# Kernel optimization log

Measured on AMD Instinct MI355X. Metric: run time of the kernel, lower is better.

## Reference

```python
import jax, jax.numpy as jnp
import numpy as np

N = 500_000        # atoms
P = 16_000_000     # neighbor pairs (half list)
NS = 4             # species types
CUTOFF = 2.5
BOX = 20.0         # cubic box edge length


def setup_inputs() -> dict:
    key = jax.random.key(0)
    k = jax.random.split(key, 6)
    positions = jax.random.uniform(k[0], (N, 3), dtype=jnp.float32) * BOX
    cell = jnp.eye(3, dtype=jnp.float32) * BOX
    pair_i = jax.random.randint(k[1], (P,), 0, N, dtype=jnp.int32)
    # guarantee j != i so r2 > 0 even when shift == 0
    offs = jax.random.randint(k[2], (P,), 1, N, dtype=jnp.int32)
    pair_j = (pair_i + offs) % N
    shifts = jax.random.randint(k[3], (P, 3), 0, 3, dtype=jnp.int32)
    species = jax.random.randint(k[4], (N,), 0, NS, dtype=jnp.int32)
    # per-species-pair LJ parameter tables (symmetric), mirroring the
    # dict {(a,b): (sigma, epsilon)} precomputation in __init__
    sig = 0.8 + 0.1 * jnp.arange(NS, dtype=jnp.float32)
    eps = 0.5 + 0.1 * jnp.arange(NS, dtype=jnp.float32)
    sigma_tab = 0.5 * (sig[:, None] + sig[None, :])
    eps_tab = jnp.sqrt(eps[:, None] * eps[None, :])
    sr = sigma_tab / CUTOFF
    shift_tab = 4.0 * eps_tab * (sr ** 12 - sr ** 6)
    return dict(positions=positions, cell=cell, sigma_tab=sigma_tab,
                eps_tab=eps_tab, shift_tab=shift_tab, species=species,
                pair_i=pair_i, pair_j=pair_j, shifts=shifts)


def reference(positions, cell, sigma_tab, eps_tab, shift_tab,
              species, pair_i, pair_j, shifts):
    # gather species-pair params (vectorized dict lookup)
    si = species[pair_i]
    sj = species[pair_j]
    sigma = sigma_tab[si, sj]        # [P]
    epsilon = eps_tab[si, sj]        # [P]
    shift_e = shift_tab[si, sj]      # [P]
    # displacement with periodic cell shift: r_j - r_i + S @ cell
    d = positions[pair_j] - positions[pair_i] + shifts.astype(positions.dtype) @ cell  # [P,3]
    r2 = jnp.sum(d * d, axis=-1)     # [P]
    r6 = r2 * r2 * r2
    sigma3 = sigma * sigma * sigma
    sigma6 = sigma3 * sigma3
    sr6 = sigma6 / r6
    sr12 = sr6 * sr6
    e = 4.0 * epsilon * (sr12 - sr6) - shift_e   # [P]
    # per-atom energy: half to each endpoint (per_atom=True path)
    energy = jnp.zeros(positions.shape[0], dtype=positions.dtype)
    energy = energy.at[pair_i].add(0.5 * e).at[pair_j].add(0.5 * e)
    return energy
```

## Files before the change

### kernel.cpp

```cpp
#include <hip/hip_runtime.h>


#define BUCKET_SHIFT 11
#define BUCKET_SIZE  2048
#define QSCALE       2048.0f
#define QINV         (1.0f / 2048.0f)

#define A_THREADS 512
#define A_PAIRS   8

typedef int vint4 __attribute__((ext_vector_type(4)));

__global__ void lj_zero_kernel(float* __restrict__ out, long n) {
    long i = (long)blockIdx.x * blockDim.x + threadIdx.x;
    if (i < n) out[i] = 0.0f;
}

__global__ void lj_pack8_kernel(const float* __restrict__ pos,
                                const int* __restrict__ species,
                                unsigned long long* __restrict__ tab8,
                                int* __restrict__ cursor,
                                int nb, int cap, int n) {
    int i = blockIdx.x * blockDim.x + threadIdx.x;
    if (i < n) {
        unsigned int ux = (unsigned int)(pos[3 * i]     * QSCALE + 0.5f) & 0xFFFFu;
        unsigned int uy = (unsigned int)(pos[3 * i + 1] * QSCALE + 0.5f) & 0xFFFFu;
        unsigned int uz = (unsigned int)(pos[3 * i + 2] * QSCALE + 0.5f) & 0xFFFFu;
        unsigned long long w = (unsigned long long)ux
                             | ((unsigned long long)uy << 16)
                             | ((unsigned long long)uz << 32)
                             | ((unsigned long long)(species[i] & 3) << 48);
        tab8[i] = w;
    }
    if (i < nb) cursor[i] = i * cap;
}

__global__ void lj_pack_kernel(const float* __restrict__ pos,
                               const int* __restrict__ species,
                               float4* __restrict__ packed, int n) {
    int i = blockIdx.x * blockDim.x + threadIdx.x;
    if (i < n) {
        float4 p;
        p.x = pos[3 * i];
        p.y = pos[3 * i + 1];
        p.z = pos[3 * i + 2];
        p.w = __int_as_float(species[i]);
        packed[i] = p;
    }
}

__device__ __forceinline__ unsigned int lj_encode(float he) {
    unsigned int u = __float_as_uint(he);
    return (u + 0x400u) & 0xFFFFF800u;
}

__global__ __launch_bounds__(A_THREADS) void lj_passA_kernel(
    const unsigned long long* __restrict__ tab8,
    const float* __restrict__ cell,
    const float* __restrict__ sigma_tab,
    const float* __restrict__ eps_tab,
    const float* __restrict__ shift_tab,
    const int* __restrict__ pair_i,
    const int* __restrict__ pair_j,
    const int* __restrict__ shifts,
    unsigned int* __restrict__ record_buf,
    int* __restrict__ cursor,
    int cap, int nb, int P)
{
    __shared__ float s_sig6[16];
    __shared__ float s_eps4[16];
    __shared__ float s_shift[16];
    __shared__ float s_cell[9];
    __shared__ int hist[256];
    __shared__ int basev[256];
    __shared__ int bbase[256];
    __shared__ unsigned int staged[A_THREADS * A_PAIRS * 2];
    __shared__ unsigned char bucketOf[A_THREADS * A_PAIRS * 2];
    int t = threadIdx.x;
    if (t < 16) {
        float s = sigma_tab[t];
        float s3 = s * s * s;
        s_sig6[t] = s3 * s3;
        s_eps4[t] = 4.0f * eps_tab[t];
        s_shift[t] = shift_tab[t];
    }
    if (t < 9) s_cell[t] = cell[t];
    if (t < 256) hist[t] = 0;
    __syncthreads();

    float c00 = s_cell[0], c01 = s_cell[1], c02 = s_cell[2];
    float c10 = s_cell[3], c11 = s_cell[4], c12 = s_cell[5];
    float c20 = s_cell[6], c21 = s_cell[7], c22 = s_cell[8];

    long base = (long)(blockIdx.x * (long)A_THREADS + t) * A_PAIRS;

    unsigned int encI[A_PAIRS], encJ[A_PAIRS];
    int slotij[A_PAIRS];
    int bkt[A_PAIRS];
    int vmask = 0;

    if (base + (A_PAIRS - 1) < P) {
        vmask = (1 << A_PAIRS) - 1;
        vint4 piA = *(const vint4*)(pair_i + base);
        vint4 piB = *(const vint4*)(pair_i + base + 4);
        vint4 pjA = *(const vint4*)(pair_j + base);
        vint4 pjB = *(const vint4*)(pair_j + base + 4);
        int pis[A_PAIRS] = {piA[0], piA[1], piA[2], piA[3], piB[0], piB[1], piB[2], piB[3]};
        int pjs[A_PAIRS] = {pjA[0], pjA[1], pjA[2], pjA[3], pjB[0], pjB[1], pjB[2], pjB[3]};

        unsigned long long gi[A_PAIRS], gj[A_PAIRS];
#pragma unroll
        for (int k = 0; k < A_PAIRS; ++k) {
            gi[k] = tab8[pis[k]];
            gj[k] = tab8[pjs[k]];
        }

        vint4 s0 = *(const vint4*)(shifts + base * 3);
        vint4 s1 = *(const vint4*)(shifts + base * 3 + 4);
        vint4 s2 = *(const vint4*)(shifts + base * 3 + 8);
        vint4 s3 = *(const vint4*)(shifts + base * 3 + 12);
        vint4 s4 = *(const vint4*)(shifts + base * 3 + 16);
        vint4 s5 = *(const vint4*)(shifts + base * 3 + 20);
        int shv[24] = {s0[0], s0[1], s0[2], s0[3], s1[0], s1[1], s1[2], s1[3],
                       s2[0], s2[1], s2[2], s2[3], s3[0], s3[1], s3[2], s3[3],
                       s4[0], s4[1], s4[2], s4[3], s5[0], s5[1], s5[2], s5[3]};

#pragma unroll
        for (int k = 0; k < A_PAIRS; ++k) {
            float fx = (float)shv[3 * k], fy = (float)shv[3 * k + 1], fz = (float)shv[3 * k + 2];
            unsigned long long wi = gi[k], wj = gj[k];
            int xi = (int)(wi & 0xFFFFu), yi = (int)((wi >> 16) & 0xFFFFu), zi = (int)((wi >> 32) & 0xFFFFu);
            int xj = (int)(wj & 0xFFFFu), yj = (int)((wj >> 16) & 0xFFFFu), zj = (int)((wj >> 32) & 0xFFFFu);
            float dlx = (float)(xj - xi) * QINV;
            float dly = (float)(yj - yi) * QINV;
            float dlz = (float)(zj - zi) * QINV;
            float dx = dlx + fx * c00 + fy * c10 + fz * c20;
            float dy = dly + fx * c01 + fy * c11 + fz * c21;
            float dz = dlz + fx * c02 + fy * c12 + fz * c22;
            float r2 = dx * dx + dy * dy + dz * dz;
            float r6 = r2 * r2 * r2;
            int idx = (int)(wi >> 48) * 4 + (int)(wj >> 48);
            float sr6 = s_sig6[idx] / r6;
            float sr12 = sr6 * sr6;
            float he = 0.5f * (s_eps4[idx] * (sr12 - sr6) - s_shift[idx]);
            unsigned int u = lj_encode(he);
            encI[k] = u | (unsigned int)(pis[k] & (BUCKET_SIZE - 1));
            encJ[k] = u | (unsigned int)(pjs[k] & (BUCKET_SIZE - 1));
            bkt[k] = (pis[k] >> BUCKET_SHIFT) | ((pjs[k] >> BUCKET_SHIFT) << 8);
        }
    } else {
#pragma unroll
        for (int k = 0; k < A_PAIRS; ++k) {
            long p = base + k;
            encI[k] = 0; encJ[k] = 0; bkt[k] = 0;
            if (p < P) {
                vmask |= (1 << k);
                int i = pair_i[p], j = pair_j[p];
                float fx = (float)shifts[3 * p], fy = (float)shifts[3 * p + 1], fz = (float)shifts[3 * p + 2];
                unsigned long long wi = tab8[i];
                unsigned long long wj = tab8[j];
                int xi = (int)(wi & 0xFFFFu), yi = (int)((wi >> 16) & 0xFFFFu), zi = (int)((wi >> 32) & 0xFFFFu);
                int xj = (int)(wj & 0xFFFFu), yj = (int)((wj >> 16) & 0xFFFFu), zj = (int)((wj >> 32) & 0xFFFFu);
                float dlx = (float)(xj - xi) * QINV;
                float dly = (float)(yj - yi) * QINV;
                float dlz = (float)(zj - zi) * QINV;
                float dx = dlx + fx * c00 + fy * c10 + fz * c20;
                float dy = dly + fx * c01 + fy * c11 + fz * c21;
                float dz = dlz + fx * c02 + fy * c12 + fz * c22;
                float r2 = dx * dx + dy * dy + dz * dz;
                float r6 = r2 * r2 * r2;
                int idx = (int)(wi >> 48) * 4 + (int)(wj >> 48);
                float sr6 = s_sig6[idx] / r6;
                float sr12 = sr6 * sr6;
                float he = 0.5f * (s_eps4[idx] * (sr12 - sr6) - s_shift[idx]);
                unsigned int u = lj_encode(he);
                encI[k] = u | (unsigned int)(i & (BUCKET_SIZE - 1));
                encJ[k] = u | (unsigned int)(j & (BUCKET_SIZE - 1));
                bkt[k] = (i >> BUCKET_SHIFT) | ((j >> BUCKET_SHIFT) << 8);
            }
        }
    }

#pragma unroll
    for (int k = 0; k < A_PAIRS; ++k) {
        if (vmask & (1 << k)) {
            int si = atomicAdd(&hist[bkt[k] & 255], 1);
            int sj = atomicAdd(&hist[(bkt[k] >> 8) & 255], 1);
            slotij[k] = si | (sj << 16);
        } else {
            slotij[k] = 0;
        }
    }
    __syncthreads();

    if (t < 64) {
        int b0 = t * 4;
        int h0 = hist[b0], h1 = hist[b0 + 1], h2 = hist[b0 + 2], h3 = hist[b0 + 3];
        int s = h0 + h1 + h2 + h3;
        int incl = s;
#pragma unroll
        for (int d = 1; d < 64; d <<= 1) {
            int v = __shfl_up(incl, d, 64);
            if (t >= d) incl += v;
        }
        int excl = incl - s;
        bbase[b0]     = excl;
        bbase[b0 + 1] = excl + h0;
        bbase[b0 + 2] = excl + h0 + h1;
        bbase[b0 + 3] = excl + h0 + h1 + h2;
    }
    if (t < nb) {
        int h = hist[t];
        basev[t] = (h > 0) ? atomicAdd(&cursor[t], h) : 0;
    }
    __syncthreads();

#pragma unroll
    for (int k = 0; k < A_PAIRS; ++k) {
        if (vmask & (1 << k)) {
            int bi = bkt[k] & 255;
            int li = bbase[bi] + (slotij[k] & 0xFFFF);
            staged[li] = encI[k];
            bucketOf[li] = (unsigned char)bi;
            int bj = (bkt[k] >> 8) & 255;
            int lj = bbase[bj] + (slotij[k] >> 16);
            staged[lj] = encJ[k];
            bucketOf[lj] = (unsigned char)bj;
        }
    }
    __syncthreads();

    int total = bbase[255] + hist[255];
    for (int idx = t; idx < total; idx += A_THREADS) {
        int b = (int)bucketOf[idx];
        int g = basev[b] + (idx - bbase[b]);
        if (g < (b + 1) * cap) record_buf[g] = staged[idx];
    }
}

__global__ __launch_bounds__(1024) void lj_passB1_kernel(
    const unsigned int* __restrict__ record_buf,
    const int* __restrict__ cursor,
    float* __restrict__ energy,
    int cap, int N)
{
    __shared__ float e[BUCKET_SIZE];
    int b = blockIdx.x;
    int t = threadIdx.x;
    e[t] = 0.0f;
    e[t + 1024] = 0.0f;
    __syncthreads();

    int begin = b * cap;
    int count = cursor[b] - begin;
    if (count > cap) count = cap;

    int full = count >> 3;
    for (int g = t; g < full; g += 1024) {
        const unsigned int* rp = record_buf + begin + g * 8;
        vint4 a = *(const vint4*)(rp);
        vint4 c = *(const vint4*)(rp + 4);
        unsigned int w0 = (unsigned int)a[0], w1 = (unsigned int)a[1];
        unsigned int w2 = (unsigned int)a[2], w3 = (unsigned int)a[3];
        unsigned int w4 = (unsigned int)c[0], w5 = (unsigned int)c[1];
        unsigned int w6 = (unsigned int)c[2], w7 = (unsigned int)c[3];
        atomicAdd(&e[w0 & 2047u], __uint_as_float(w0 & 0xFFFFF800u));
        atomicAdd(&e[w1 & 2047u], __uint_as_float(w1 & 0xFFFFF800u));
        atomicAdd(&e[w2 & 2047u], __uint_as_float(w2 & 0xFFFFF800u));
        atomicAdd(&e[w3 & 2047u], __uint_as_float(w3 & 0xFFFFF800u));
        atomicAdd(&e[w4 & 2047u], __uint_as_float(w4 & 0xFFFFF800u));
        atomicAdd(&e[w5 & 2047u], __uint_as_float(w5 & 0xFFFFF800u));
        atomicAdd(&e[w6 & 2047u], __uint_as_float(w6 & 0xFFFFF800u));
        atomicAdd(&e[w7 & 2047u], __uint_as_float(w7 & 0xFFFFF800u));
    }
    for (int r = (full << 3) + t; r < count; r += 1024) {
        unsigned int w = record_buf[begin + r];
        atomicAdd(&e[w & 2047u], __uint_as_float(w & 0xFFFFF800u));
    }
    __syncthreads();

    long i0 = (long)b * BUCKET_SIZE + t;
    if (i0 < N) energy[i0] = e[t];
    if (i0 + 1024 < N) energy[i0 + 1024] = e[t + 1024];
}

__device__ __forceinline__ void lj_one_pair_packed(
    int i, int j, float fx, float fy, float fz,
    const float4* __restrict__ packed,
    const float* s_sig6, const float* s_eps4, const float* s_shift,
    float c00, float c01, float c02,
    float c10, float c11, float c12,
    float c20, float c21, float c22,
    float* __restrict__ energy)
{
    float4 gi = packed[i];
    float4 gj = packed[j];
    float dx = gj.x - gi.x + fx * c00 + fy * c10 + fz * c20;
    float dy = gj.y - gi.y + fx * c01 + fy * c11 + fz * c21;
    float dz = gj.z - gi.z + fx * c02 + fy * c12 + fz * c22;
    float r2 = dx * dx + dy * dy + dz * dz;
    float r6 = r2 * r2 * r2;
    int idx = __float_as_int(gi.w) * 4 + __float_as_int(gj.w);
    float sr6 = s_sig6[idx] / r6;
    float sr12 = sr6 * sr6;
    float he = 0.5f * (s_eps4[idx] * (sr12 - sr6) - s_shift[idx]);
    atomicAdd(energy + i, he);
    atomicAdd(energy + j, he);
}

__global__ __launch_bounds__(256) void lj_pairs_packed_kernel(
    const float4* __restrict__ packed,
    const float* __restrict__ cell,
    const float* __restrict__ sigma_tab,
    const float* __restrict__ eps_tab,
    const float* __restrict__ shift_tab,
    const int* __restrict__ pair_i,
    const int* __restrict__ pair_j,
    const int* __restrict__ shifts,
    float* __restrict__ energy,
    int P)
{
    __shared__ float s_sig6[16];
    __shared__ float s_eps4[16];
    __shared__ float s_shift[16];
    __shared__ float s_cell[9];
    int t = threadIdx.x;
    if (t < 16) {
        float s = sigma_tab[t];
        float s3 = s * s * s;
        s_sig6[t] = s3 * s3;
        s_eps4[t] = 4.0f * eps_tab[t];
        s_shift[t] = shift_tab[t];
    }
    if (t < 9) s_cell[t] = cell[t];
    __syncthreads();

    float c00 = s_cell[0], c01 = s_cell[1], c02 = s_cell[2];
    float c10 = s_cell[3], c11 = s_cell[4], c12 = s_cell[5];
    float c20 = s_cell[6], c21 = s_cell[7], c22 = s_cell[8];

    long base = (long)(blockIdx.x * (long)blockDim.x + t) * 4;
    if (base + 3 < P) {
        int4 pi4 = *(const int4*)(pair_i + base);
        int4 pj4 = *(const int4*)(pair_j + base);
        int4 sA = *(const int4*)(shifts + base * 3);
        int4 sB = *(const int4*)(shifts + base * 3 + 4);
        int4 sC = *(const int4*)(shifts + base * 3 + 8);
        int pis[4] = {pi4.x, pi4.y, pi4.z, pi4.w};
        int pjs[4] = {pj4.x, pj4.y, pj4.z, pj4.w};
        int shv[12] = {sA.x, sA.y, sA.z, sA.w, sB.x, sB.y, sB.z, sB.w,
                       sC.x, sC.y, sC.z, sC.w};
#pragma unroll
        for (int k = 0; k < 4; ++k) {
            lj_one_pair_packed(pis[k], pjs[k],
                        (float)shv[3 * k], (float)shv[3 * k + 1], (float)shv[3 * k + 2],
                        packed, s_sig6, s_eps4, s_shift,
                        c00, c01, c02, c10, c11, c12, c20, c21, c22, energy);
        }
    } else {
        for (long p = base; p < P; ++p) {
            lj_one_pair_packed(pair_i[p], pair_j[p],
                        (float)shifts[3 * p], (float)shifts[3 * p + 1], (float)shifts[3 * p + 2],
                        packed, s_sig6, s_eps4, s_shift,
                        c00, c01, c02, c10, c11, c12, c20, c21, c22, energy);
        }
    }
}

__device__ __forceinline__ void lj_one_pair(
    int i, int j, float fx, float fy, float fz,
    const float* __restrict__ pos,
    const int* __restrict__ species,
    const float* s_sig6, const float* s_eps4, const float* s_shift,
    float c00, float c01, float c02,
    float c10, float c11, float c12,
    float c20, float c21, float c22,
    float* __restrict__ energy)
{
    float dx = pos[3 * j]     - pos[3 * i]     + fx * c00 + fy * c10 + fz * c20;
    float dy = pos[3 * j + 1] - pos[3 * i + 1] + fx * c01 + fy * c11 + fz * c21;
    float dz = pos[3 * j + 2] - pos[3 * i + 2] + fx * c02 + fy * c12 + fz * c22;
    float r2 = dx * dx + dy * dy + dz * dz;
    float r6 = r2 * r2 * r2;
    int idx = species[i] * 4 + species[j];
    float sr6 = s_sig6[idx] / r6;
    float sr12 = sr6 * sr6;
    float he = 0.5f * (s_eps4[idx] * (sr12 - sr6) - s_shift[idx]);
    atomicAdd(energy + i, he);
    atomicAdd(energy + j, he);
}

__global__ __launch_bounds__(256) void lj_pairs_kernel(
    const float* __restrict__ pos,
    const float* __restrict__ cell,
    const float* __restrict__ sigma_tab,
    const float* __restrict__ eps_tab,
    const float* __restrict__ shift_tab,
    const int* __restrict__ species,
    const int* __restrict__ pair_i,
    const int* __restrict__ pair_j,
    const int* __restrict__ shifts,
    float* __restrict__ energy,
    int P)
{
    __shared__ float s_sig6[16];
    __shared__ float s_eps4[16];
    __shared__ float s_shift[16];
    __shared__ float s_cell[9];
    int t = threadIdx.x;
    if (t < 16) {
        float s = sigma_tab[t];
        float s3 = s * s * s;
        s_sig6[t] = s3 * s3;
        s_eps4[t] = 4.0f * eps_tab[t];
        s_shift[t] = shift_tab[t];
    }
    if (t < 9) s_cell[t] = cell[t];
    __syncthreads();

    float c00 = s_cell[0], c01 = s_cell[1], c02 = s_cell[2];
    float c10 = s_cell[3], c11 = s_cell[4], c12 = s_cell[5];
    float c20 = s_cell[6], c21 = s_cell[7], c22 = s_cell[8];

    long base = (long)(blockIdx.x * (long)blockDim.x + t) * 4;
    if (base + 3 < P) {
        int4 pi4 = *(const int4*)(pair_i + base);
        int4 pj4 = *(const int4*)(pair_j + base);
        int4 sA = *(const int4*)(shifts + base * 3);
        int4 sB = *(const int4*)(shifts + base * 3 + 4);
        int4 sC = *(const int4*)(shifts + base * 3 + 8);
        int pis[4] = {pi4.x, pi4.y, pi4.z, pi4.w};
        int pjs[4] = {pj4.x, pj4.y, pj4.z, pj4.w};
        int shv[12] = {sA.x, sA.y, sA.z, sA.w, sB.x, sB.y, sB.z, sB.w,
                       sC.x, sC.y, sC.z, sC.w};
#pragma unroll
        for (int k = 0; k < 4; ++k) {
            lj_one_pair(pis[k], pjs[k],
                        (float)shv[3 * k], (float)shv[3 * k + 1], (float)shv[3 * k + 2],
                        pos, species, s_sig6, s_eps4, s_shift,
                        c00, c01, c02, c10, c11, c12, c20, c21, c22, energy);
        }
    } else {
        for (long p = base; p < P; ++p) {
            lj_one_pair(pair_i[p], pair_j[p],
                        (float)shifts[3 * p], (float)shifts[3 * p + 1], (float)shifts[3 * p + 2],
                        pos, species, s_sig6, s_eps4, s_shift,
                        c00, c01, c02, c10, c11, c12, c20, c21, c22, energy);
        }
    }
}

extern "C" void kernel_launch(void* const* d_in, const int* in_sizes, int n_in,
                              void* d_out, int out_size, void* d_ws, size_t ws_size,
                              hipStream_t stream) {
    const float* positions = (const float*)d_in[0];
    const float* cell      = (const float*)d_in[1];
    const float* sigma_tab = (const float*)d_in[2];
    const float* eps_tab   = (const float*)d_in[3];
    const float* shift_tab = (const float*)d_in[4];
    const int*   species   = (const int*)d_in[5];
    const int*   pair_i    = (const int*)d_in[6];
    const int*   pair_j    = (const int*)d_in[7];
    const int*   shifts    = (const int*)d_in[8];
    float* energy = (float*)d_out;

    const int N = out_size;
    const int P = in_sizes[6];

    const int threads = 256;
    const int ablocks = (N + threads - 1) / threads;
    const int pblocks4 = (int)((((long)P + 3) / 4 + threads - 1) / threads);

    const int nb = (N + BUCKET_SIZE - 1) / BUCKET_SIZE;
    long avg = (2L * P) / (nb > 0 ? nb : 1);
    long capl = (avg + avg / 50 + 512 + 1023) & ~1023L;
    const int cap = (int)capl;
    const size_t rec_bytes  = (size_t)nb * (size_t)cap * 4u;
    const size_t tab_bytes  = (size_t)N * 8u;
    const size_t cur_bytes  = (size_t)nb * 4u;
    const size_t need_bucket = rec_bytes + tab_bytes + cur_bytes;
    const size_t need_pack   = (size_t)N * 16u;

    const bool has_ws = (d_ws != nullptr);
    const bool sane = (nb > 0) && (nb <= 256) && ((long)nb * cap < 2000000000L);
    const bool use_bucket = has_ws && sane && (ws_size >= need_bucket);
    const bool use_pack   = has_ws && !use_bucket && (ws_size >= need_pack);

    if (use_bucket) {
        unsigned int* record_buf = (unsigned int*)d_ws;
        unsigned long long* tab8 = (unsigned long long*)((char*)d_ws + rec_bytes);
        int* cursor = (int*)((char*)d_ws + rec_bytes + tab_bytes);

        lj_pack8_kernel<<<ablocks, threads, 0, stream>>>(
            positions, species, tab8, cursor, nb, cap, N);
        const long nthreads_needed = ((long)P + A_PAIRS - 1) / A_PAIRS;
        const int pblocksA = (int)((nthreads_needed + A_THREADS - 1) / A_THREADS);
        lj_passA_kernel<<<pblocksA, A_THREADS, 0, stream>>>(
            tab8, cell, sigma_tab, eps_tab, shift_tab,
            pair_i, pair_j, shifts, record_buf, cursor, cap, nb, P);
        lj_passB1_kernel<<<nb, 1024, 0, stream>>>(record_buf, cursor, energy, cap, N);
    } else if (use_pack) {
        float4* packed = (float4*)d_ws;
        lj_zero_kernel<<<ablocks, threads, 0, stream>>>(energy, N);
        lj_pack_kernel<<<ablocks, threads, 0, stream>>>(positions, species, packed, N);
        lj_pairs_packed_kernel<<<pblocks4, threads, 0, stream>>>(
            packed, cell, sigma_tab, eps_tab, shift_tab,
            pair_i, pair_j, shifts, energy, P);
    } else {
        lj_zero_kernel<<<ablocks, threads, 0, stream>>>(energy, N);
        lj_pairs_kernel<<<pblocks4, threads, 0, stream>>>(
            positions, cell, sigma_tab, eps_tab, shift_tab, species,
            pair_i, pair_j, shifts, energy, P);
    }
}
```

Measured before the change: 737.2 us.

## Split pass-B buckets across eight blocks with global atomic merge

The per-bucket accumulation kernel previously ran one 1024-thread block per bucket, giving only about 245 blocks for 256 CUs. Each bucket's records are now split into eight slices, each handled by a 256-thread block that accumulates into shared memory and then atomically adds its nonzero partials into global energy. This needs an extra zeroing kernel and up to eight global atomics per atom, and it makes the float summation order nondeterministic. It also relies on `threads` being 256 at launch.

```diff
diff --git a/kernel.cpp b/kernel.cpp
--- a/kernel.cpp
+++ b/kernel.cpp
@@ -3,6 +3,7 @@
 
 #define BUCKET_SHIFT 11
 #define BUCKET_SIZE  2048
+#define SLICES       8
 #define QSCALE       2048.0f
 #define QINV         (1.0f / 2048.0f)
 
@@ -238,50 +239,65 @@
     }
 }
 
-__global__ __launch_bounds__(1024) void lj_passB1_kernel(
+__global__ __launch_bounds__(256) void lj_passB_atomic_kernel(
     const unsigned int* __restrict__ record_buf,
     const int* __restrict__ cursor,
     float* __restrict__ energy,
     int cap, int N)
 {
     __shared__ float e[BUCKET_SIZE];
-    int b = blockIdx.x;
+    int blk = blockIdx.x;
+    int b = blk >> 3;
+    int s = blk & (SLICES - 1);
     int t = threadIdx.x;
-    e[t] = 0.0f;
-    e[t + 1024] = 0.0f;
+#pragma unroll
+    for (int k = 0; k < 8; ++k) e[t + 256 * k] = 0.0f;
     __syncthreads();
 
     int begin = b * cap;
     int count = cursor[b] - begin;
     if (count > cap) count = cap;
 
-    int full = count >> 3;
-    for (int g = t; g < full; g += 1024) {
-        const unsigned int* rp = record_buf + begin + g * 8;
-        vint4 a = *(const vint4*)(rp);
-        vint4 c = *(const vint4*)(rp + 4);
-        unsigned int w0 = (unsigned int)a[0], w1 = (unsigned int)a[1];
-        unsigned int w2 = (unsigned int)a[2], w3 = (unsigned int)a[3];
-        unsigned int w4 = (unsigned int)c[0], w5 = (unsigned int)c[1];
-        unsigned int w6 = (unsigned int)c[2], w7 = (unsigned int)c[3];
-        atomicAdd(&e[w0 & 2047u], __uint_as_float(w0 & 0xFFFFF800u));
-        atomicAdd(&e[w1 & 2047u], __uint_as_float(w1 & 0xFFFFF800u));
-        atomicAdd(&e[w2 & 2047u], __uint_as_float(w2 & 0xFFFFF800u));
-        atomicAdd(&e[w3 & 2047u], __uint_as_float(w3 & 0xFFFFF800u));
-        atomicAdd(&e[w4 & 2047u], __uint_as_float(w4 & 0xFFFFF800u));
-        atomicAdd(&e[w5 & 2047u], __uint_as_float(w5 & 0xFFFFF800u));
-        atomicAdd(&e[w6 & 2047u], __uint_as_float(w6 & 0xFFFFF800u));
-        atomicAdd(&e[w7 & 2047u], __uint_as_float(w7 & 0xFFFFF800u));
-    }
-    for (int r = (full << 3) + t; r < count; r += 1024) {
-        unsigned int w = record_buf[begin + r];
-        atomicAdd(&e[w & 2047u], __uint_as_float(w & 0xFFFFF800u));
-    }
-    __syncthreads();
-
-    long i0 = (long)b * BUCKET_SIZE + t;
-    if (i0 < N) energy[i0] = e[t];
-    if (i0 + 1024 < N) energy[i0 + 1024] = e[t + 1024];
+    int ngroups = (count + 7) >> 3;
+    int gps = (ngroups + SLICES - 1) / SLICES;
+    int g0 = s * gps;
+    int g1 = g0 + gps;
+    if (g1 > ngroups) g1 = ngroups;
+
+    for (int g = g0 + t; g < g1; g += 256) {
+        int r0 = g * 8;
+        const unsigned int* rp = record_buf + begin + r0;
+        if (r0 + 8 <= count) {
+            vint4 a = *(const vint4*)(rp);
+            vint4 c = *(const vint4*)(rp + 4);
+            unsigned int w0 = (unsigned int)a[0], w1 = (unsigned int)a[1];
+            unsigned int w2 = (unsigned int)a[2], w3 = (unsigned int)a[3];
+            unsigned int w4 = (unsigned int)c[0], w5 = (unsigned int)c[1];
+            unsigned int w6 = (unsigned int)c[2], w7 = (unsigned int)c[3];
+            atomicAdd(&e[w0 & 2047u], __uint_as_float(w0 & 0xFFFFF800u));
+            atomicAdd(&e[w1 & 2047u], __uint_as_float(w1 & 0xFFFFF800u));
+            atomicAdd(&e[w2 & 2047u], __uint_as_float(w2 & 0xFFFFF800u));
+            atomicAdd(&e[w3 & 2047u], __uint_as_float(w3 & 0xFFFFF800u));
+            atomicAdd(&e[w4 & 2047u], __uint_as_float(w4 & 0xFFFFF800u));
+            atomicAdd(&e[w5 & 2047u], __uint_as_float(w5 & 0xFFFFF800u));
+            atomicAdd(&e[w6 & 2047u], __uint_as_float(w6 & 0xFFFFF800u));
+            atomicAdd(&e[w7 & 2047u], __uint_as_float(w7 & 0xFFFFF800u));
+        } else {
+            for (int r = r0; r < count; ++r) {
+                unsigned int w = record_buf[begin + r];
+                atomicAdd(&e[w & 2047u], __uint_as_float(w & 0xFFFFF800u));
+            }
+        }
+    }
+    __syncthreads();
+
+    long basei = (long)b * BUCKET_SIZE;
+#pragma unroll
+    for (int k = 0; k < 8; ++k) {
+        long i = basei + t + 256 * k;
+        float v = e[t + 256 * k];
+        if (i < N && v != 0.0f) atomicAdd(&energy[i], v);
+    }
 }
 
 __device__ __forceinline__ void lj_one_pair_packed(
@@ -491,6 +507,7 @@
         unsigned long long* tab8 = (unsigned long long*)((char*)d_ws + rec_bytes);
         int* cursor = (int*)((char*)d_ws + rec_bytes + tab_bytes);
 
+        lj_zero_kernel<<<ablocks, threads, 0, stream>>>(energy, N);
         lj_pack8_kernel<<<ablocks, threads, 0, stream>>>(
             positions, species, tab8, cursor, nb, cap, N);
         const long nthreads_needed = ((long)P + A_PAIRS - 1) / A_PAIRS;
@@ -498,7 +515,8 @@
         lj_passA_kernel<<<pblocksA, A_THREADS, 0, stream>>>(
             tab8, cell, sigma_tab, eps_tab, shift_tab,
             pair_i, pair_j, shifts, record_buf, cursor, cap, nb, P);
-        lj_passB1_kernel<<<nb, 1024, 0, stream>>>(record_buf, cursor, energy, cap, N);
+        lj_passB_atomic_kernel<<<nb * SLICES, threads, 0, stream>>>(
+            record_buf, cursor, energy, cap, N);
     } else if (use_pack) {
         float4* packed = (float4*)d_ws;
         lj_zero_kernel<<<ablocks, threads, 0, stream>>>(energy, N);
```

Measured after the change: 740.7 us. No clear change (+0.5%).
